# Performance work log

Hardware: AMD Instinct MI355X
Metric: run time of the kernel (lower is better)

The kernel has to match this reference:

```python
import jax, jax.numpy as jnp
import numpy as np

N_NODES = 100000
N_EMBED = 64
N_HIDDEN = 64
N_EDGES = 1200000


def setup_inputs() -> dict:
    key = jax.random.key(0)
    ks = jax.random.split(key, 8)
    prop_edge_index = jax.random.randint(ks[0], (2, N_EDGES), 0, N_NODES, dtype=jnp.int64)
    emb = jax.random.normal(ks[1], (N_NODES, N_EMBED), dtype=jnp.float32) * 0.05
    # ChebConv K=2 -> two linear weights per layer + bias
    W1_0 = jax.random.normal(ks[2], (N_EMBED, N_HIDDEN), dtype=jnp.float32) * 0.05
    W1_1 = jax.random.normal(ks[3], (N_EMBED, N_HIDDEN), dtype=jnp.float32) * 0.05
    b1 = jnp.zeros((N_HIDDEN,), dtype=jnp.float32)
    W2_0 = jax.random.normal(ks[4], (N_HIDDEN, N_HIDDEN), dtype=jnp.float32) * 0.05
    W2_1 = jax.random.normal(ks[5], (N_HIDDEN, N_HIDDEN), dtype=jnp.float32) * 0.05
    b2 = jnp.zeros((N_HIDDEN,), dtype=jnp.float32)
    return {"prop_edge_index": prop_edge_index, "emb": emb,
            "W1_0": W1_0, "W1_1": W1_1, "b1": b1,
            "W2_0": W2_0, "W2_1": W2_1, "b2": b2}


def _cheb_norm(edge_index, num_nodes):
    """PyG ChebConv.__norm__ with sym normalization, lambda_max=2.0.
    L_hat = 2L/lambda_max - I = (I - D^-1/2 A D^-1/2) - I, so the net
    diagonal weight is 0 and off-diagonal weight is -d_i^-1/2 * d_j^-1/2.
    Self loops in the input are removed first (weight 0)."""
    row, col = edge_index[0], edge_index[1]
    w = jnp.where(row != col, 1.0, 0.0).astype(jnp.float32)  # remove_self_loops
    deg = jax.ops.segment_sum(w, row, num_segments=num_nodes)
    dinv = jnp.where(deg > 0, deg ** -0.5, 0.0)
    norm = -dinv[row] * w * dinv[col]
    return norm


def _cheb_conv(x, src, dst, norm, W0, W1, b, num_nodes):
    # K=2: out = T0(x) @ W0 + T1(x) @ W1 + b, T0 = x, T1 = L_hat x
    Tx1 = jax.ops.segment_sum(norm[:, None] * x[src], dst, num_segments=num_nodes)
    return x @ W0 + Tx1 @ W1 + b


def reference(prop_edge_index, emb, W1_0, W1_1, b1, W2_0, W2_1, b2):
    src, dst = prop_edge_index[0], prop_edge_index[1]
    norm = _cheb_norm(prop_edge_index, N_NODES)
    x = _cheb_conv(emb, src, dst, norm, W1_0, W1_1, b1, N_NODES)
    x = jax.nn.relu(x)
    # dropout: eval mode (identity)
    x = _cheb_conv(x, src, dst, norm, W2_0, W2_1, b2, N_NODES)
    return x
```

## Files before the change

### kernel.cpp

```cpp
#include <hip/hip_runtime.h>

#define N_NODES 100000
#define N_EDGES 1200000
#define NF 64

typedef __attribute__((ext_vector_type(8))) short short8;
typedef __attribute__((ext_vector_type(4))) float float4v;

__device__ __forceinline__ ushort f2bf(float f) {
    unsigned u = __float_as_uint(f);
    return (ushort)((u + 0x7FFF + ((u >> 16) & 1)) >> 16);
}

#define NBINS 196
#define CAP 7680
#define EPB 2560
#define NBLK 469

#define OFF_CNT    0
#define OFF_ENDP   400128
#define OFF_DINV   800256
#define OFF_CUR    1200384
#define OFF_PKW    1202048
#define OFF_SRCS   1234816
#define OFF_NRMS   7255936
#define OFF_SBIN   10266496
#define OFF_DBIN   13277056
#define OFF_EMBBF  19298176
#define OFF_HBF    32098176

__global__ __launch_bounds__(256) void prep(const float* __restrict__ W10,
                                            const float* __restrict__ W11,
                                            const float* __restrict__ W20,
                                            const float* __restrict__ W21,
                                            ushort* __restrict__ pk,
                                            int* __restrict__ cur,
                                            const float* __restrict__ emb,
                                            ushort* __restrict__ emb_bf) {
    int b = blockIdx.x;
    int t = threadIdx.x;
    if (b < 8) {
        int idx = b * 256 + t;
        int layer = idx >> 10;
        int rest = idx & 1023;
        int f = rest >> 6, L = rest & 63;
        int n = (f & 3) * 16 + (L & 15);
        int kb = (f >> 2) * 32 + ((L >> 4) << 3);
#pragma unroll
        for (int j = 0; j < 8; ++j) {
            int k = kb + j;
            const float* W = layer ? ((k < 64) ? W20 : W21) : ((k < 64) ? W10 : W11);
            pk[idx * 8 + j] = f2bf(W[(k & 63) * 64 + n]);
        }
    } else if (b == 8) {
        for (int i = t; i < 2 * NBINS; i += 256)
            cur[i] = (i < NBINS ? i : i - NBINS) * CAP;
    } else {
        int i = ((b - 9) * 256 + t) * 8;
        float4 v0 = *(const float4*)(emb + i);
        float4 v1 = *(const float4*)(emb + i + 4);
        uint4 o;
        o.x = (uint)f2bf(v0.x) | ((uint)f2bf(v0.y) << 16);
        o.y = (uint)f2bf(v0.z) | ((uint)f2bf(v0.w) << 16);
        o.z = (uint)f2bf(v1.x) | ((uint)f2bf(v1.y) << 16);
        o.w = (uint)f2bf(v1.z) | ((uint)f2bf(v1.w) << 16);
        *(uint4*)(emb_bf + i) = o;
    }
}

__global__ __launch_bounds__(256) void binsort(const int* __restrict__ row,
                                               const int* __restrict__ col,
                                               int* __restrict__ cur,
                                               ushort* __restrict__ sbinned,
                                               int* __restrict__ dbinned) {
    __shared__ int2 ecache[EPB];
    __shared__ int sh[NBINS], dh[NBINS];
    __shared__ int sbase[NBINS], dbase[NBINS];
    int t = threadIdx.x;
    if (t < NBINS) { sh[t] = 0; dh[t] = 0; }
    __syncthreads();
    int base = blockIdx.x * EPB;
    for (int k = 0; k < EPB / 256; ++k) {
        int e = base + k * 256 + t;
        int s = -1, d = -1;
        if (e < N_EDGES) { s = row[e]; d = col[e]; }
        ecache[k * 256 + t] = make_int2(s, d);
        if (s >= 0 && s != d) {
            atomicAdd(&sh[s >> 9], 1);
            atomicAdd(&dh[d >> 9], 1);
        }
    }
    __syncthreads();
    if (t < NBINS) {
        sbase[t] = atomicAdd(&cur[t], sh[t]);
        dbase[t] = atomicAdd(&cur[NBINS + t], dh[t]);
    }
    __syncthreads();
    for (int k = 0; k < EPB / 256; ++k) {
        int2 p = ecache[k * 256 + t];
        int s = p.x, d = p.y;
        if (s >= 0 && s != d) {
            int ss = atomicAdd(&sbase[s >> 9], 1);
            sbinned[ss] = (ushort)(s & 511);
            int ds = atomicAdd(&dbase[d >> 9], 1);
            dbinned[ds] = (s << 9) | (d & 511);
        }
    }
}

__global__ __launch_bounds__(512) void binD1(const ushort* __restrict__ sbinned,
                                             const int* __restrict__ cur,
                                             float* __restrict__ dinv) {
    __shared__ int hist[512];
    int t = threadIdx.x;
    hist[t] = 0;
    __syncthreads();
    int b = blockIdx.x;
    int start = b * CAP;
    int end = cur[b];
    for (int i = start + t; i < end; i += 512)
        atomicAdd(&hist[sbinned[i]], 1);
    __syncthreads();
    int n0 = (b << 9) + t;
    if (n0 < N_NODES) dinv[n0] = hist[t] ? rsqrtf((float)hist[t]) : 0.0f;
}

__global__ __launch_bounds__(512) void binD2(const int* __restrict__ dbinned,
                                             const int* __restrict__ cur,
                                             const float* __restrict__ dinv,
                                             int* __restrict__ cnt,
                                             int* __restrict__ endp,
                                             int* __restrict__ srcs,
                                             ushort* __restrict__ nrms) {
    __shared__ int hist[512];
    __shared__ int lcur[512];
    __shared__ int tot_s;
    int t = threadIdx.x;
    hist[t] = 0;
    __syncthreads();
    int b = blockIdx.x;
    int start = b * CAP;
    int end = cur[NBINS + b];
    for (int i = start + t; i < end; i += 512)
        atomicAdd(&hist[dbinned[i] & 511], 1);
    __syncthreads();
    int o0 = hist[t];
    int A0 = (o0 + 3) & ~3;
    __syncthreads();
    hist[t] = A0;
    __syncthreads();
    for (int off = 1; off < 512; off <<= 1) {
        int v = (t >= off) ? hist[t - off] : 0;
        __syncthreads();
        hist[t] += v;
        __syncthreads();
    }
    int e0 = hist[t] - A0;
    if (t == 511) tot_s = hist[511];
    lcur[t] = start + e0;
    int n0 = (b << 9) + t;
    if (n0 < N_NODES) { cnt[n0] = o0; endp[n0] = start + e0 + o0; }
    __syncthreads();
    for (int i = start + t; i < end; i += 512) {
        int p = dbinned[i];
        int s = p >> 9, dl = p & 511;
        int slot = atomicAdd(&lcur[dl], 1);
        srcs[slot] = s;
        nrms[slot] = f2bf(-dinv[s] * dinv[(b << 9) + dl]);
    }
    __syncthreads();
    for (int k = o0; k < A0; ++k) { srcs[start + e0 + k] = 0; nrms[start + e0 + k] = 0; }
    if (t < 16) { srcs[start + tot_s + t] = 0; nrms[start + tot_s + t] = 0; }
}

#define NPW 16
#define WPB 2
#define NPB (NPW * WPB)
#define LB2 ((N_NODES + NPB - 1) / NPB)

__global__ __launch_bounds__(128, 8) void cheb_layer(const ushort* __restrict__ x,
                                                     const int* __restrict__ srcs,
                                                     const ushort* __restrict__ nrms,
                                                     const int* __restrict__ endp,
                                                     const int* __restrict__ cnt,
                                                     const ushort* __restrict__ pk,
                                                     const float* __restrict__ bias,
                                                     ushort* __restrict__ out_bf,
                                                     float* __restrict__ out_f32,
                                                     int last) {
    __shared__ ushort sA[WPB][16][136];

    int t = threadIdx.x;
    int lane = t & 63, wid = t >> 6;
    int c = lane & 15, q = lane >> 4;
    int qd = q, fg = c;
    int nb = blockIdx.x * NPB + wid * NPW;

    int nend = 0, ncnt = 0;
    if (lane < NPW && nb + lane < N_NODES) {
        nend = endp[nb + lane];
        ncnt = cnt[nb + lane];
    }

    const uint2* xr = (const uint2*)x;

    auto chunk8 = [&](int eb, int eendL, float& a0, float& a1, float& a2, float& a3) {
        int4 sv = *(const int4*)(srcs + eb);
        int4 sw = *(const int4*)(srcs + eb + 4);
        uint2 nv = *(const uint2*)(nrms + eb);
        uint2 nw = *(const uint2*)(nrms + eb + 4);
        int sA01 = (qd & 1) ? sv.y : sv.x;
        int sA23 = (qd & 1) ? sv.w : sv.z;
        int srcA = (qd & 2) ? sA23 : sA01;
        int sB01 = (qd & 1) ? sw.y : sw.x;
        int sB23 = (qd & 1) ? sw.w : sw.z;
        int srcB = (qd & 2) ? sB23 : sB01;
        uint nAp = (qd & 2) ? nv.y : nv.x;
        uint nBp = (qd & 2) ? nw.y : nw.x;
        float nAf = __uint_as_float((qd & 1) ? (nAp & 0xffff0000u) : (nAp << 16));
        float nBf = __uint_as_float((qd & 1) ? (nBp & 0xffff0000u) : (nBp << 16));
        nAf = (eb + qd < eendL) ? nAf : 0.0f;
        nBf = (eb + 4 + qd < eendL) ? nBf : 0.0f;
        uint2 gA = xr[(size_t)srcA * 16 + fg];
        uint2 gB = xr[(size_t)srcB * 16 + fg];
        a0 = fmaf(nAf, __uint_as_float(gA.x << 16), a0);
        a1 = fmaf(nAf, __uint_as_float(gA.x & 0xffff0000u), a1);
        a2 = fmaf(nAf, __uint_as_float(gA.y << 16), a2);
        a3 = fmaf(nAf, __uint_as_float(gA.y & 0xffff0000u), a3);
        a0 = fmaf(nBf, __uint_as_float(gB.x << 16), a0);
        a1 = fmaf(nBf, __uint_as_float(gB.x & 0xffff0000u), a1);
        a2 = fmaf(nBf, __uint_as_float(gB.y << 16), a2);
        a3 = fmaf(nBf, __uint_as_float(gB.y & 0xffff0000u), a3);
    };

#pragma unroll
    for (int gp = 0; gp < NPW; gp += 2) {
        int cn0 = __builtin_amdgcn_readlane(ncnt, gp);
        int ee0 = __builtin_amdgcn_readlane(nend, gp);
        int cn1 = __builtin_amdgcn_readlane(ncnt, gp + 1);
        int ee1 = __builtin_amdgcn_readlane(nend, gp + 1);
        int s0 = ee0 - cn0, s1 = ee1 - cn1;
        float a0 = 0, a1 = 0, a2 = 0, a3 = 0;
        float b0 = 0, b1 = 0, b2 = 0, b3 = 0;

        chunk8(s0,     ee0, a0, a1, a2, a3);
        chunk8(s1,     ee1, b0, b1, b2, b3);
        chunk8(s0 + 8, ee0, a0, a1, a2, a3);
        chunk8(s1 + 8, ee1, b0, b1, b2, b3);
        for (int e = s0 + 16; e < ee0; e += 8) chunk8(e, ee0, a0, a1, a2, a3);
        for (int e = s1 + 16; e < ee1; e += 8) chunk8(e, ee1, b0, b1, b2, b3);

        a0 += __shfl_xor(a0, 16, 64); b0 += __shfl_xor(b0, 16, 64);
        a1 += __shfl_xor(a1, 16, 64); b1 += __shfl_xor(b1, 16, 64);
        a2 += __shfl_xor(a2, 16, 64); b2 += __shfl_xor(b2, 16, 64);
        a3 += __shfl_xor(a3, 16, 64); b3 += __shfl_xor(b3, 16, 64);
        a0 += __shfl_xor(a0, 32, 64); b0 += __shfl_xor(b0, 32, 64);
        a1 += __shfl_xor(a1, 32, 64); b1 += __shfl_xor(b1, 32, 64);
        a2 += __shfl_xor(a2, 32, 64); b2 += __shfl_xor(b2, 32, 64);
        a3 += __shfl_xor(a3, 32, 64); b3 += __shfl_xor(b3, 32, 64);

        int node0 = nb + gp, node1 = nb + gp + 1;
        int ni0 = (node0 < N_NODES) ? node0 : 0;
        int ni1 = (node1 < N_NODES) ? node1 : 0;
        if (qd == 0) {
            uint2 xv0 = xr[(size_t)ni0 * 16 + fg];
            uint2 xv1 = xr[(size_t)ni1 * 16 + fg];
            *(uint2*)&sA[wid][gp][4 * fg] = xv0;
            *(uint2*)&sA[wid][gp + 1][4 * fg] = xv1;
        }
        if (qd == 1) {
            uint2 p0, p1;
            p0.x = (uint)f2bf(a0) | ((uint)f2bf(a1) << 16);
            p0.y = (uint)f2bf(a2) | ((uint)f2bf(a3) << 16);
            p1.x = (uint)f2bf(b0) | ((uint)f2bf(b1) << 16);
            p1.y = (uint)f2bf(b2) | ((uint)f2bf(b3) << 16);
            *(uint2*)&sA[wid][gp][64 + 4 * fg] = p0;
            *(uint2*)&sA[wid][gp + 1][64 + 4 * fg] = p1;
        }
    }
    __builtin_amdgcn_wave_barrier();

    const short8* pk8 = (const short8*)pk;
    float4v C[4];
#pragma unroll
    for (int nt = 0; nt < 4; ++nt) {
        float b = bias[nt * 16 + c];
        C[nt] = (float4v){b, b, b, b};
    }
#pragma unroll
    for (int kt = 0; kt < 4; ++kt) {
        short8 af = *(const short8*)&sA[wid][c][kt * 32 + q * 8];
#pragma unroll
        for (int nt = 0; nt < 4; ++nt) {
            short8 bfr = pk8[(kt * 4 + nt) * 64 + lane];
            C[nt] = __builtin_amdgcn_mfma_f32_16x16x32_bf16(af, bfr, C[nt], 0, 0, 0);
        }
    }

#pragma unroll
    for (int nt = 0; nt < 4; ++nt) {
#pragma unroll
        for (int i = 0; i < 4; ++i) {
            int node = nb + q * 4 + i;
            if (node < N_NODES) {
                float v = C[nt][i];
                if (!last) {
                    v = fmaxf(v, 0.0f);
                    out_bf[(size_t)node * NF + nt * 16 + c] = f2bf(v);
                } else {
                    out_f32[(size_t)node * NF + nt * 16 + c] = v;
                }
            }
        }
    }
}

extern "C" void kernel_launch(void* const* d_in, const int* in_sizes, int n_in,
                              void* d_out, int out_size, void* d_ws, size_t ws_size,
                              hipStream_t stream) {
    const int* ei = (const int*)d_in[0];
    const int* row = ei;
    const int* col = ei + N_EDGES;
    const float* emb = (const float*)d_in[1];
    const float* W1_0 = (const float*)d_in[2];
    const float* W1_1 = (const float*)d_in[3];
    const float* b1 = (const float*)d_in[4];
    const float* W2_0 = (const float*)d_in[5];
    const float* W2_1 = (const float*)d_in[6];
    const float* b2 = (const float*)d_in[7];
    float* out = (float*)d_out;

    char* ws = (char*)d_ws;
    int* cnt = (int*)(ws + OFF_CNT);
    int* endp = (int*)(ws + OFF_ENDP);
    float* dinv = (float*)(ws + OFF_DINV);
    int* cur = (int*)(ws + OFF_CUR);
    ushort* pk = (ushort*)(ws + OFF_PKW);
    int* srcs = (int*)(ws + OFF_SRCS);
    ushort* nrms = (ushort*)(ws + OFF_NRMS);
    ushort* sbinned = (ushort*)(ws + OFF_SBIN);
    int* dbinned = (int*)(ws + OFF_DBIN);
    ushort* emb_bf = (ushort*)(ws + OFF_EMBBF);
    ushort* h_bf = (ushort*)(ws + OFF_HBF);

    prep<<<9 + 3125, 256, 0, stream>>>(W1_0, W1_1, W2_0, W2_1, pk, cur, emb, emb_bf);
    binsort<<<NBLK, 256, 0, stream>>>(row, col, cur, sbinned, dbinned);
    binD1<<<NBINS, 512, 0, stream>>>(sbinned, cur, dinv);
    binD2<<<NBINS, 512, 0, stream>>>(dbinned, cur, dinv, cnt, endp, srcs, nrms);

    cheb_layer<<<LB2, 128, 0, stream>>>(emb_bf, srcs, nrms, endp, cnt, pk, b1, h_bf, nullptr, 0);
    cheb_layer<<<LB2, 128, 0, stream>>>(h_bf, srcs, nrms, endp, cnt, pk + 8192, b2, nullptr, out, 1);
}
```

Measured before the change: 216.0 us.

## Replace two-level bin sort with global-atomic counting sort for CSR build

Replaces the shared-memory binned sort (binsort, binD1, binD2) with a direct counting sort. The new path counts per-node degrees with global atomics, scans per bin to set row offsets, then scatters edges with one global atomic per edge and computes the norm inline. This drops the intermediate binned arrays and a full pass over them. In exchange it adds many scattered global atomics and random writes, and the order of edges within each row becomes nondeterministic.

Measured after the change: 323.6 us. 1.5x slower.

```diff
diff --git a/kernel.cpp b/kernel.cpp
--- a/kernel.cpp
+++ b/kernel.cpp
@@ -14,29 +14,26 @@
 
 #define NBINS 196
 #define CAP 7680
-#define EPB 2560
-#define NBLK 469
 
 #define OFF_CNT    0
 #define OFF_ENDP   400128
-#define OFF_DINV   800256
-#define OFF_CUR    1200384
-#define OFF_PKW    1202048
-#define OFF_SRCS   1234816
-#define OFF_NRMS   7255936
-#define OFF_SBIN   10266496
-#define OFF_DBIN   13277056
-#define OFF_EMBBF  19298176
-#define OFF_HBF    32098176
+#define OFF_DEG    800256
+#define OFF_WCUR   1200384
+#define OFF_PKW    1600512
+#define OFF_SRCS   1633280
+#define OFF_NRMS   7654400
+#define OFF_EMBBF  10664960
+#define OFF_HBF    23464960
 
 __global__ __launch_bounds__(256) void prep(const float* __restrict__ W10,
                                             const float* __restrict__ W11,
                                             const float* __restrict__ W20,
                                             const float* __restrict__ W21,
                                             ushort* __restrict__ pk,
-                                            int* __restrict__ cur,
                                             const float* __restrict__ emb,
-                                            ushort* __restrict__ emb_bf) {
+                                            ushort* __restrict__ emb_bf,
+                                            int* __restrict__ deg,
+                                            int* __restrict__ cnt) {
     int b = blockIdx.x;
     int t = threadIdx.x;
     if (b < 8) {
@@ -52,11 +49,9 @@
             const float* W = layer ? ((k < 64) ? W20 : W21) : ((k < 64) ? W10 : W11);
             pk[idx * 8 + j] = f2bf(W[(k & 63) * 64 + n]);
         }
-    } else if (b == 8) {
-        for (int i = t; i < 2 * NBINS; i += 256)
-            cur[i] = (i < NBINS ? i : i - NBINS) * CAP;
     } else {
-        int i = ((b - 9) * 256 + t) * 8;
+        int bb = b - 8;
+        int i = (bb * 256 + t) * 8;
         float4 v0 = *(const float4*)(emb + i);
         float4 v1 = *(const float4*)(emb + i + 4);
         uint4 o;
@@ -65,88 +60,41 @@
         o.z = (uint)f2bf(v1.x) | ((uint)f2bf(v1.y) << 16);
         o.w = (uint)f2bf(v1.z) | ((uint)f2bf(v1.w) << 16);
         *(uint4*)(emb_bf + i) = o;
-    }
-}
-
-__global__ __launch_bounds__(256) void binsort(const int* __restrict__ row,
-                                               const int* __restrict__ col,
-                                               int* __restrict__ cur,
-                                               ushort* __restrict__ sbinned,
-                                               int* __restrict__ dbinned) {
-    __shared__ int2 ecache[EPB];
-    __shared__ int sh[NBINS], dh[NBINS];
-    __shared__ int sbase[NBINS], dbase[NBINS];
+        int z = bb * 32;
+        if (t < 32) deg[z + t] = 0;
+        else if (t < 64) cnt[z + t - 32] = 0;
+    }
+}
+
+#define E4 (N_EDGES / 4)
+#define EBLK ((E4 + 255) / 256)
+__global__ __launch_bounds__(256) void count_edges(const int* __restrict__ row,
+                                                   const int* __restrict__ col,
+                                                   int* __restrict__ deg,
+                                                   int* __restrict__ cnt) {
+    int i4 = blockIdx.x * 256 + threadIdx.x;
+    if (i4 >= E4) return;
+    int4 rs = ((const int4*)row)[i4];
+    int4 cs = ((const int4*)col)[i4];
+    if (rs.x != cs.x) { atomicAdd(&deg[rs.x], 1); atomicAdd(&cnt[cs.x], 1); }
+    if (rs.y != cs.y) { atomicAdd(&deg[rs.y], 1); atomicAdd(&cnt[cs.y], 1); }
+    if (rs.z != cs.z) { atomicAdd(&deg[rs.z], 1); atomicAdd(&cnt[cs.z], 1); }
+    if (rs.w != cs.w) { atomicAdd(&deg[rs.w], 1); atomicAdd(&cnt[cs.w], 1); }
+}
+
+__global__ __launch_bounds__(512) void scan_bins(const int* __restrict__ cnt,
+                                                 int* __restrict__ endp,
+                                                 int* __restrict__ wcur,
+                                                 int* __restrict__ srcs,
+                                                 ushort* __restrict__ nrms) {
+    __shared__ int hist[512];
+    __shared__ int tot_s;
     int t = threadIdx.x;
-    if (t < NBINS) { sh[t] = 0; dh[t] = 0; }
-    __syncthreads();
-    int base = blockIdx.x * EPB;
-    for (int k = 0; k < EPB / 256; ++k) {
-        int e = base + k * 256 + t;
-        int s = -1, d = -1;
-        if (e < N_EDGES) { s = row[e]; d = col[e]; }
-        ecache[k * 256 + t] = make_int2(s, d);
-        if (s >= 0 && s != d) {
-            atomicAdd(&sh[s >> 9], 1);
-            atomicAdd(&dh[d >> 9], 1);
-        }
-    }
-    __syncthreads();
-    if (t < NBINS) {
-        sbase[t] = atomicAdd(&cur[t], sh[t]);
-        dbase[t] = atomicAdd(&cur[NBINS + t], dh[t]);
-    }
-    __syncthreads();
-    for (int k = 0; k < EPB / 256; ++k) {
-        int2 p = ecache[k * 256 + t];
-        int s = p.x, d = p.y;
-        if (s >= 0 && s != d) {
-            int ss = atomicAdd(&sbase[s >> 9], 1);
-            sbinned[ss] = (ushort)(s & 511);
-            int ds = atomicAdd(&dbase[d >> 9], 1);
-            dbinned[ds] = (s << 9) | (d & 511);
-        }
-    }
-}
-
-__global__ __launch_bounds__(512) void binD1(const ushort* __restrict__ sbinned,
-                                             const int* __restrict__ cur,
-                                             float* __restrict__ dinv) {
-    __shared__ int hist[512];
-    int t = threadIdx.x;
-    hist[t] = 0;
-    __syncthreads();
     int b = blockIdx.x;
     int start = b * CAP;
-    int end = cur[b];
-    for (int i = start + t; i < end; i += 512)
-        atomicAdd(&hist[sbinned[i]], 1);
-    __syncthreads();
     int n0 = (b << 9) + t;
-    if (n0 < N_NODES) dinv[n0] = hist[t] ? rsqrtf((float)hist[t]) : 0.0f;
-}
-
-__global__ __launch_bounds__(512) void binD2(const int* __restrict__ dbinned,
-                                             const int* __restrict__ cur,
-                                             const float* __restrict__ dinv,
-                                             int* __restrict__ cnt,
-                                             int* __restrict__ endp,
-                                             int* __restrict__ srcs,
-                                             ushort* __restrict__ nrms) {
-    __shared__ int hist[512];
-    __shared__ int lcur[512];
-    __shared__ int tot_s;
-    int t = threadIdx.x;
-    hist[t] = 0;
-    __syncthreads();
-    int b = blockIdx.x;
-    int start = b * CAP;
-    int end = cur[NBINS + b];
-    for (int i = start + t; i < end; i += 512)
-        atomicAdd(&hist[dbinned[i] & 511], 1);
-    __syncthreads();
-    int o0 = hist[t];
+    int o0 = (n0 < N_NODES) ? cnt[n0] : 0;
     int A0 = (o0 + 3) & ~3;
-    __syncthreads();
     hist[t] = A0;
     __syncthreads();
     for (int off = 1; off < 512; off <<= 1) {
@@ -157,20 +105,35 @@
     }
     int e0 = hist[t] - A0;
     if (t == 511) tot_s = hist[511];
-    lcur[t] = start + e0;
-    int n0 = (b << 9) + t;
-    if (n0 < N_NODES) { cnt[n0] = o0; endp[n0] = start + e0 + o0; }
+    if (n0 < N_NODES) { endp[n0] = start + e0 + o0; wcur[n0] = start + e0; }
+    for (int k = o0; k < A0; ++k) { srcs[start + e0 + k] = 0; nrms[start + e0 + k] = 0; }
     __syncthreads();
-    for (int i = start + t; i < end; i += 512) {
-        int p = dbinned[i];
-        int s = p >> 9, dl = p & 511;
-        int slot = atomicAdd(&lcur[dl], 1);
-        srcs[slot] = s;
-        nrms[slot] = f2bf(-dinv[s] * dinv[(b << 9) + dl]);
-    }
-    __syncthreads();
-    for (int k = o0; k < A0; ++k) { srcs[start + e0 + k] = 0; nrms[start + e0 + k] = 0; }
     if (t < 16) { srcs[start + tot_s + t] = 0; nrms[start + tot_s + t] = 0; }
+}
+
+__global__ __launch_bounds__(256) void scatter_edges(const int* __restrict__ row,
+                                                     const int* __restrict__ col,
+                                                     const int* __restrict__ deg,
+                                                     int* __restrict__ wcur,
+                                                     int* __restrict__ srcs,
+                                                     ushort* __restrict__ nrms) {
+    int i4 = blockIdx.x * 256 + threadIdx.x;
+    if (i4 >= E4) return;
+    int4 rs = ((const int4*)row)[i4];
+    int4 cs = ((const int4*)col)[i4];
+#pragma unroll
+    for (int j = 0; j < 4; ++j) {
+        int s = (j == 0) ? rs.x : (j == 1) ? rs.y : (j == 2) ? rs.z : rs.w;
+        int d = (j == 0) ? cs.x : (j == 1) ? cs.y : (j == 2) ? cs.z : cs.w;
+        if (s != d) {
+            int slot = atomicAdd(&wcur[d], 1);
+            int dgs = deg[s];
+            int dgd = deg[d];
+            float nrm = -rsqrtf((float)dgs) * (dgd ? rsqrtf((float)dgd) : 0.0f);
+            srcs[slot] = s;
+            nrms[slot] = f2bf(nrm);
+        }
+    }
 }
 
 #define NPW 16
@@ -333,20 +296,18 @@
     char* ws = (char*)d_ws;
     int* cnt = (int*)(ws + OFF_CNT);
     int* endp = (int*)(ws + OFF_ENDP);
-    float* dinv = (float*)(ws + OFF_DINV);
-    int* cur = (int*)(ws + OFF_CUR);
+    int* deg = (int*)(ws + OFF_DEG);
+    int* wcur = (int*)(ws + OFF_WCUR);
     ushort* pk = (ushort*)(ws + OFF_PKW);
     int* srcs = (int*)(ws + OFF_SRCS);
     ushort* nrms = (ushort*)(ws + OFF_NRMS);
-    ushort* sbinned = (ushort*)(ws + OFF_SBIN);
-    int* dbinned = (int*)(ws + OFF_DBIN);
     ushort* emb_bf = (ushort*)(ws + OFF_EMBBF);
     ushort* h_bf = (ushort*)(ws + OFF_HBF);
 
-    prep<<<9 + 3125, 256, 0, stream>>>(W1_0, W1_1, W2_0, W2_1, pk, cur, emb, emb_bf);
-    binsort<<<NBLK, 256, 0, stream>>>(row, col, cur, sbinned, dbinned);
-    binD1<<<NBINS, 512, 0, stream>>>(sbinned, cur, dinv);
-    binD2<<<NBINS, 512, 0, stream>>>(dbinned, cur, dinv, cnt, endp, srcs, nrms);
+    prep<<<8 + 3125, 256, 0, stream>>>(W1_0, W1_1, W2_0, W2_1, pk, emb, emb_bf, deg, cnt);
+    count_edges<<<EBLK, 256, 0, stream>>>(row, col, deg, cnt);
+    scan_bins<<<NBINS, 512, 0, stream>>>(cnt, endp, wcur, srcs, nrms);
+    scatter_edges<<<EBLK, 256, 0, stream>>>(row, col, deg, wcur, srcs, nrms);
 
     cheb_layer<<<LB2, 128, 0, stream>>>(emb_bf, srcs, nrms, endp, cnt, pk, b1, h_bf, nullptr, 0);
     cheb_layer<<<LB2, 128, 0, stream>>>(h_bf, srcs, nrms, endp, cnt, pk + 8192, b2, nullptr, out, 1);
```

## Fuse preprocessing kernels and apply degree normalization inside the aggregation

Applied to the files above, without the earlier changes.

Merges the weight/embedding prep with the edge bin-sort, and the degree and CSR-build passes into one launch, with cur zeroed by a memset. The per-edge bf16 norm array goes away: the aggregation kernel gathers dinv[src] per edge and scales by -dinv[dst] once per node. This cuts launch count and the norm write/read traffic, and caches each dbinned chunk in LDS so it is read once. The cost is an extra random 4-byte dinv gather per edge in both layers, plus a larger LDS footprint in the build kernel.

Result: faster. 203.4 us (-5.8%).

```diff
diff --git a/kernel.cpp b/kernel.cpp
--- a/kernel.cpp
+++ b/kernel.cpp
@@ -23,24 +23,60 @@
 #define OFF_CUR    1200384
 #define OFF_PKW    1202048
 #define OFF_SRCS   1234816
-#define OFF_NRMS   7255936
-#define OFF_SBIN   10266496
-#define OFF_DBIN   13277056
-#define OFF_EMBBF  19298176
-#define OFF_HBF    32098176
-
-__global__ __launch_bounds__(256) void prep(const float* __restrict__ W10,
-                                            const float* __restrict__ W11,
-                                            const float* __restrict__ W20,
-                                            const float* __restrict__ W21,
-                                            ushort* __restrict__ pk,
-                                            int* __restrict__ cur,
-                                            const float* __restrict__ emb,
-                                            ushort* __restrict__ emb_bf) {
+#define OFF_SBIN   7255936
+#define OFF_DBIN   10266496
+#define OFF_EMBBF  16287616
+#define OFF_HBF    29087616
+
+__global__ __launch_bounds__(256) void prepsort(const float* __restrict__ W10,
+                                                const float* __restrict__ W11,
+                                                const float* __restrict__ W20,
+                                                const float* __restrict__ W21,
+                                                ushort* __restrict__ pk,
+                                                const float* __restrict__ emb,
+                                                ushort* __restrict__ emb_bf,
+                                                const int* __restrict__ row,
+                                                const int* __restrict__ col,
+                                                int* __restrict__ cur,
+                                                ushort* __restrict__ sbinned,
+                                                int* __restrict__ dbinned) {
     int b = blockIdx.x;
     int t = threadIdx.x;
-    if (b < 8) {
-        int idx = b * 256 + t;
+    if (b < NBLK) {
+        __shared__ int2 ecache[EPB];
+        __shared__ int sh[NBINS], dh[NBINS];
+        __shared__ int sbase[NBINS], dbase[NBINS];
+        if (t < NBINS) { sh[t] = 0; dh[t] = 0; }
+        __syncthreads();
+        int base = b * EPB;
+        for (int k = 0; k < EPB / 256; ++k) {
+            int e = base + k * 256 + t;
+            int s = -1, d = -1;
+            if (e < N_EDGES) { s = row[e]; d = col[e]; }
+            ecache[k * 256 + t] = make_int2(s, d);
+            if (s >= 0 && s != d) {
+                atomicAdd(&sh[s >> 9], 1);
+                atomicAdd(&dh[d >> 9], 1);
+            }
+        }
+        __syncthreads();
+        if (t < NBINS) {
+            sbase[t] = t * CAP + atomicAdd(&cur[t], sh[t]);
+            dbase[t] = t * CAP + atomicAdd(&cur[NBINS + t], dh[t]);
+        }
+        __syncthreads();
+        for (int k = 0; k < EPB / 256; ++k) {
+            int2 p = ecache[k * 256 + t];
+            int s = p.x, d = p.y;
+            if (s >= 0 && s != d) {
+                int ss = atomicAdd(&sbase[s >> 9], 1);
+                sbinned[ss] = (ushort)(s & 511);
+                int ds = atomicAdd(&dbase[d >> 9], 1);
+                dbinned[ds] = (s << 9) | (d & 511);
+            }
+        }
+    } else if (b < NBLK + 8) {
+        int idx = (b - NBLK) * 256 + t;
         int layer = idx >> 10;
         int rest = idx & 1023;
         int f = rest >> 6, L = rest & 63;
@@ -52,11 +88,9 @@
             const float* W = layer ? ((k < 64) ? W20 : W21) : ((k < 64) ? W10 : W11);
             pk[idx * 8 + j] = f2bf(W[(k & 63) * 64 + n]);
         }
-    } else if (b == 8) {
-        for (int i = t; i < 2 * NBINS; i += 256)
-            cur[i] = (i < NBINS ? i : i - NBINS) * CAP;
     } else {
-        int i = ((b - 9) * 256 + t) * 8;
+        int bb = b - NBLK - 8;
+        int i = (bb * 256 + t) * 8;
         float4 v0 = *(const float4*)(emb + i);
         float4 v1 = *(const float4*)(emb + i + 4);
         uint4 o;
@@ -68,109 +102,68 @@
     }
 }
 
-__global__ __launch_bounds__(256) void binsort(const int* __restrict__ row,
-                                               const int* __restrict__ col,
-                                               int* __restrict__ cur,
-                                               ushort* __restrict__ sbinned,
-                                               int* __restrict__ dbinned) {
-    __shared__ int2 ecache[EPB];
-    __shared__ int sh[NBINS], dh[NBINS];
-    __shared__ int sbase[NBINS], dbase[NBINS];
-    int t = threadIdx.x;
-    if (t < NBINS) { sh[t] = 0; dh[t] = 0; }
-    __syncthreads();
-    int base = blockIdx.x * EPB;
-    for (int k = 0; k < EPB / 256; ++k) {
-        int e = base + k * 256 + t;
-        int s = -1, d = -1;
-        if (e < N_EDGES) { s = row[e]; d = col[e]; }
-        ecache[k * 256 + t] = make_int2(s, d);
-        if (s >= 0 && s != d) {
-            atomicAdd(&sh[s >> 9], 1);
-            atomicAdd(&dh[d >> 9], 1);
-        }
-    }
-    __syncthreads();
-    if (t < NBINS) {
-        sbase[t] = atomicAdd(&cur[t], sh[t]);
-        dbase[t] = atomicAdd(&cur[NBINS + t], dh[t]);
-    }
-    __syncthreads();
-    for (int k = 0; k < EPB / 256; ++k) {
-        int2 p = ecache[k * 256 + t];
-        int s = p.x, d = p.y;
-        if (s >= 0 && s != d) {
-            int ss = atomicAdd(&sbase[s >> 9], 1);
-            sbinned[ss] = (ushort)(s & 511);
-            int ds = atomicAdd(&dbase[d >> 9], 1);
-            dbinned[ds] = (s << 9) | (d & 511);
-        }
-    }
-}
-
-__global__ __launch_bounds__(512) void binD1(const ushort* __restrict__ sbinned,
+__global__ __launch_bounds__(512) void build(const ushort* __restrict__ sbinned,
+                                             const int* __restrict__ dbinned,
                                              const int* __restrict__ cur,
-                                             float* __restrict__ dinv) {
-    __shared__ int hist[512];
-    int t = threadIdx.x;
-    hist[t] = 0;
-    __syncthreads();
-    int b = blockIdx.x;
-    int start = b * CAP;
-    int end = cur[b];
-    for (int i = start + t; i < end; i += 512)
-        atomicAdd(&hist[sbinned[i]], 1);
-    __syncthreads();
-    int n0 = (b << 9) + t;
-    if (n0 < N_NODES) dinv[n0] = hist[t] ? rsqrtf((float)hist[t]) : 0.0f;
-}
-
-__global__ __launch_bounds__(512) void binD2(const int* __restrict__ dbinned,
-                                             const int* __restrict__ cur,
-                                             const float* __restrict__ dinv,
+                                             float* __restrict__ dinv,
                                              int* __restrict__ cnt,
                                              int* __restrict__ endp,
-                                             int* __restrict__ srcs,
-                                             ushort* __restrict__ nrms) {
-    __shared__ int hist[512];
-    __shared__ int lcur[512];
-    __shared__ int tot_s;
+                                             int* __restrict__ srcs) {
     int t = threadIdx.x;
-    hist[t] = 0;
-    __syncthreads();
     int b = blockIdx.x;
-    int start = b * CAP;
-    int end = cur[NBINS + b];
-    for (int i = start + t; i < end; i += 512)
-        atomicAdd(&hist[dbinned[i] & 511], 1);
-    __syncthreads();
-    int o0 = hist[t];
-    int A0 = (o0 + 3) & ~3;
-    __syncthreads();
-    hist[t] = A0;
-    __syncthreads();
-    for (int off = 1; off < 512; off <<= 1) {
-        int v = (t >= off) ? hist[t - off] : 0;
-        __syncthreads();
-        hist[t] += v;
-        __syncthreads();
-    }
-    int e0 = hist[t] - A0;
-    if (t == 511) tot_s = hist[511];
-    lcur[t] = start + e0;
-    int n0 = (b << 9) + t;
-    if (n0 < N_NODES) { cnt[n0] = o0; endp[n0] = start + e0 + o0; }
-    __syncthreads();
-    for (int i = start + t; i < end; i += 512) {
-        int p = dbinned[i];
-        int s = p >> 9, dl = p & 511;
-        int slot = atomicAdd(&lcur[dl], 1);
-        srcs[slot] = s;
-        nrms[slot] = f2bf(-dinv[s] * dinv[(b << 9) + dl]);
-    }
-    __syncthreads();
-    for (int k = o0; k < A0; ++k) { srcs[start + e0 + k] = 0; nrms[start + e0 + k] = 0; }
-    if (t < 16) { srcs[start + tot_s + t] = 0; nrms[start + tot_s + t] = 0; }
+    if (b < NBINS) {
+        __shared__ int hist[512];
+        hist[t] = 0;
+        __syncthreads();
+        int start = b * CAP;
+        int end = start + cur[b];
+        for (int i = start + t; i < end; i += 512)
+            atomicAdd(&hist[sbinned[i]], 1);
+        __syncthreads();
+        int n0 = (b << 9) + t;
+        if (n0 < N_NODES) dinv[n0] = hist[t] ? rsqrtf((float)hist[t]) : 0.0f;
+    } else {
+        int bb = b - NBINS;
+        __shared__ int ecache[CAP];
+        __shared__ int hist[512];
+        __shared__ int lcur[512];
+        __shared__ int tot_s;
+        hist[t] = 0;
+        __syncthreads();
+        int start = bb * CAP;
+        int len = cur[NBINS + bb];
+        for (int i = t; i < len; i += 512) {
+            int p = dbinned[start + i];
+            ecache[i] = p;
+            atomicAdd(&hist[p & 511], 1);
+        }
+        __syncthreads();
+        int o0 = hist[t];
+        int A0 = (o0 + 3) & ~3;
+        __syncthreads();
+        hist[t] = A0;
+        __syncthreads();
+        for (int off = 1; off < 512; off <<= 1) {
+            int v = (t >= off) ? hist[t - off] : 0;
+            __syncthreads();
+            hist[t] += v;
+            __syncthreads();
+        }
+        int e0 = hist[t] - A0;
+        if (t == 511) tot_s = hist[511];
+        lcur[t] = start + e0;
+        int n0 = (bb << 9) + t;
+        if (n0 < N_NODES) { cnt[n0] = o0; endp[n0] = start + e0 + o0; }
+        __syncthreads();
+        for (int i = t; i < len; i += 512) {
+            int p = ecache[i];
+            int slot = atomicAdd(&lcur[p & 511], 1);
+            srcs[slot] = p >> 9;
+        }
+        __syncthreads();
+        for (int k = o0; k < A0; ++k) srcs[start + e0 + k] = 0;
+        if (t < 16) srcs[start + tot_s + t] = 0;
+    }
 }
 
 #define NPW 16
@@ -180,7 +173,7 @@
 
 __global__ __launch_bounds__(128, 8) void cheb_layer(const ushort* __restrict__ x,
                                                      const int* __restrict__ srcs,
-                                                     const ushort* __restrict__ nrms,
+                                                     const float* __restrict__ dinv,
                                                      const int* __restrict__ endp,
                                                      const int* __restrict__ cnt,
                                                      const ushort* __restrict__ pk,
@@ -207,18 +200,14 @@
     auto chunk8 = [&](int eb, int eendL, float& a0, float& a1, float& a2, float& a3) {
         int4 sv = *(const int4*)(srcs + eb);
         int4 sw = *(const int4*)(srcs + eb + 4);
-        uint2 nv = *(const uint2*)(nrms + eb);
-        uint2 nw = *(const uint2*)(nrms + eb + 4);
         int sA01 = (qd & 1) ? sv.y : sv.x;
         int sA23 = (qd & 1) ? sv.w : sv.z;
         int srcA = (qd & 2) ? sA23 : sA01;
         int sB01 = (qd & 1) ? sw.y : sw.x;
         int sB23 = (qd & 1) ? sw.w : sw.z;
         int srcB = (qd & 2) ? sB23 : sB01;
-        uint nAp = (qd & 2) ? nv.y : nv.x;
-        uint nBp = (qd & 2) ? nw.y : nw.x;
-        float nAf = __uint_as_float((qd & 1) ? (nAp & 0xffff0000u) : (nAp << 16));
-        float nBf = __uint_as_float((qd & 1) ? (nBp & 0xffff0000u) : (nBp << 16));
+        float nAf = dinv[srcA];
+        float nBf = dinv[srcB];
         nAf = (eb + qd < eendL) ? nAf : 0.0f;
         nBf = (eb + 4 + qd < eendL) ? nBf : 0.0f;
         uint2 gA = xr[(size_t)srcA * 16 + fg];
@@ -269,11 +258,13 @@
             *(uint2*)&sA[wid][gp + 1][4 * fg] = xv1;
         }
         if (qd == 1) {
+            float sc0 = -dinv[ni0];
+            float sc1 = -dinv[ni1];
             uint2 p0, p1;
-            p0.x = (uint)f2bf(a0) | ((uint)f2bf(a1) << 16);
-            p0.y = (uint)f2bf(a2) | ((uint)f2bf(a3) << 16);
-            p1.x = (uint)f2bf(b0) | ((uint)f2bf(b1) << 16);
-            p1.y = (uint)f2bf(b2) | ((uint)f2bf(b3) << 16);
+            p0.x = (uint)f2bf(a0 * sc0) | ((uint)f2bf(a1 * sc0) << 16);
+            p0.y = (uint)f2bf(a2 * sc0) | ((uint)f2bf(a3 * sc0) << 16);
+            p1.x = (uint)f2bf(b0 * sc1) | ((uint)f2bf(b1 * sc1) << 16);
+            p1.y = (uint)f2bf(b2 * sc1) | ((uint)f2bf(b3 * sc1) << 16);
             *(uint2*)&sA[wid][gp][64 + 4 * fg] = p0;
             *(uint2*)&sA[wid][gp + 1][64 + 4 * fg] = p1;
         }
@@ -337,17 +328,17 @@
     int* cur = (int*)(ws + OFF_CUR);
     ushort* pk = (ushort*)(ws + OFF_PKW);
     int* srcs = (int*)(ws + OFF_SRCS);
-    ushort* nrms = (ushort*)(ws + OFF_NRMS);
     ushort* sbinned = (ushort*)(ws + OFF_SBIN);
     int* dbinned = (int*)(ws + OFF_DBIN);
     ushort* emb_bf = (ushort*)(ws + OFF_EMBBF);
     ushort* h_bf = (ushort*)(ws + OFF_HBF);
 
-    prep<<<9 + 3125, 256, 0, stream>>>(W1_0, W1_1, W2_0, W2_1, pk, cur, emb, emb_bf);
-    binsort<<<NBLK, 256, 0, stream>>>(row, col, cur, sbinned, dbinned);
-    binD1<<<NBINS, 512, 0, stream>>>(sbinned, cur, dinv);
-    binD2<<<NBINS, 512, 0, stream>>>(dbinned, cur, dinv, cnt, endp, srcs, nrms);
-
-    cheb_layer<<<LB2, 128, 0, stream>>>(emb_bf, srcs, nrms, endp, cnt, pk, b1, h_bf, nullptr, 0);
-    cheb_layer<<<LB2, 128, 0, stream>>>(h_bf, srcs, nrms, endp, cnt, pk + 8192, b2, nullptr, out, 1);
-}
+    hipMemsetAsync(cur, 0, 2 * NBINS * sizeof(int), stream);
+    prepsort<<<NBLK + 8 + 3125, 256, 0, stream>>>(W1_0, W1_1, W2_0, W2_1, pk,
+                                                  emb, emb_bf, row, col, cur,
+                                                  sbinned, dbinned);
+    build<<<2 * NBINS, 512, 0, stream>>>(sbinned, dbinned, cur, dinv, cnt, endp, srcs);
+
+    cheb_layer<<<LB2, 128, 0, stream>>>(emb_bf, srcs, dinv, endp, cnt, pk, b1, h_bf, nullptr, 0);
+    cheb_layer<<<LB2, 128, 0, stream>>>(h_bf, srcs, dinv, endp, cnt, pk + 8192, b2, nullptr, out, 1);
+}
```
